# Optimization experiments

Measured on AMD Instinct MI355X. Metric: run time of the kernel, lower is better.

Reference implementation:

```python
import jax, jax.numpy as jnp
import numpy as np

N = 50000
NUM_NEIGHBORS = 16
E = N * NUM_NEIGHBORS
NDIM_IN, EDIM, NDIM_OUT = 128, 64, 128


def setup_inputs() -> dict:
    key = jax.random.key(0)
    k1, k2, k3, k4, k5, k6, k7 = jax.random.split(key, 7)
    nfeats = jax.random.normal(k1, (N, 1, NDIM_IN), dtype=jnp.float32)
    efeats = jax.random.normal(k2, (E, 1, EDIM), dtype=jnp.float32)
    W_msg = jax.random.normal(k3, (NDIM_OUT, NDIM_IN + EDIM), dtype=jnp.float32) * 0.05
    b_msg = jax.random.normal(k4, (NDIM_OUT,), dtype=jnp.float32) * 0.05
    W_apply = jax.random.normal(k5, (NDIM_OUT, NDIM_IN + NDIM_OUT), dtype=jnp.float32) * 0.05
    b_apply = jax.random.normal(k6, (NDIM_OUT,), dtype=jnp.float32) * 0.05
    src_idx = jax.random.randint(k7, (E,), 0, N, dtype=jnp.int32)
    # sampled graph: each node is the destination of exactly NUM_NEIGHBORS edges
    dst_idx = jnp.repeat(jnp.arange(N, dtype=jnp.int32), NUM_NEIGHBORS)
    return {"nfeats": nfeats, "efeats": efeats, "W_msg": W_msg, "b_msg": b_msg,
            "W_apply": W_apply, "b_apply": b_apply, "src_idx": src_idx, "dst_idx": dst_idx}


def reference(nfeats, efeats, W_msg, b_msg, W_apply, b_apply, src_idx, dst_idx):
    n = nfeats.shape[0]
    # message: W_msg(cat([src_h, edge_h], -1))  -> [E, 1, ndim_out]
    src_h = nfeats[src_idx]                                   # [E,1,Din] gather
    msg_in = jnp.concatenate([src_h, efeats], axis=-1)        # [E,1,Din+Edim]
    m = jnp.einsum('eid,od->eio', msg_in, W_msg) + b_msg      # [E,1,Dout]
    # mean aggregation over incoming edges per destination node
    msum = jax.ops.segment_sum(m[:, 0, :], dst_idx, num_segments=n)   # [N,Dout]
    cnt = jax.ops.segment_sum(jnp.ones((m.shape[0],), m.dtype), dst_idx, num_segments=n)
    h_neigh = (msum / jnp.maximum(cnt, 1.0)[:, None])[:, None, :]     # [N,1,Dout]
    # apply: relu(W_apply(cat([nfeats, h_neigh], -1)))
    app_in = jnp.concatenate([nfeats, h_neigh], axis=-1)      # [N,1,Din+Dout]
    h_new = jax.nn.relu(jnp.einsum('nid,od->nio', app_in, W_apply) + b_apply)
    return h_new
```

## Files before the change

### kernel.cpp

```cpp
#include <hip/hip_runtime.h>

#define N_NODES 50000
#define NN 16
#define K_FUSED 320
#define NP 50048

typedef __attribute__((ext_vector_type(8))) short bfrag8;
typedef __attribute__((ext_vector_type(4))) float facc4;

__device__ __forceinline__ unsigned short f2bf(float f) {
    unsigned int u = __builtin_bit_cast(unsigned int, f);
    u = (u + 0x7fffu + ((u >> 16) & 1u)) >> 16;
    return (unsigned short)u;
}

__global__ void wfuse_kernel(const float* __restrict__ W_msg,
                             const float* __restrict__ b_msg,
                             const float* __restrict__ W_apply,
                             const float* __restrict__ b_apply,
                             unsigned short* __restrict__ Wf,
                             float* __restrict__ bias_f) {
    __shared__ float sWa[128];
    const int o = blockIdx.x;
    const int tid = threadIdx.x;
    if (tid < 128) sWa[tid] = W_apply[o * 256 + 128 + tid];
    __syncthreads();
    if (tid < 128) Wf[o * K_FUSED + tid] = f2bf(W_apply[o * 256 + tid]);
    if (tid < 192) {
        float acc = 0.f;
        #pragma unroll 8
        for (int p = 0; p < 128; ++p) acc += sWa[p] * W_msg[p * 192 + tid];
        Wf[o * K_FUSED + 128 + tid] = f2bf(acc);
    } else if (tid == 192) {
        float acc = b_apply[o];
        for (int p = 0; p < 128; ++p) acc += sWa[p] * b_msg[p];
        bias_f[o] = acc;
    }
}

__global__ __launch_bounds__(256)
void prep_kernel(const float* __restrict__ nfeats,
                 const float* __restrict__ efeats,
                 const int* __restrict__ src_idx,
                 unsigned short* __restrict__ X) {
    const int wave = threadIdx.x >> 6;
    const int lane = threadIdx.x & 63;
    const int n = blockIdx.x * 4 + wave;
    if (n >= N_NODES) return;
    const long e0 = (long)n * NN;

    float s0 = 0.f, s1 = 0.f;
    float tacc = 0.f;
    #pragma unroll
    for (int j = 0; j < NN; ++j) {
        const int src = src_idx[e0 + j];
        const float2 v = *(const float2*)(nfeats + (long)src * 128 + 2 * lane);
        s0 += v.x; s1 += v.y;
        tacc += efeats[(e0 + j) * 64 + lane];
    }
    const float inv = 1.f / 16.f;
    s0 *= inv; s1 *= inv; tacc *= inv;

    const float2 xv = *(const float2*)(nfeats + (long)n * 128 + 2 * lane);
    unsigned short* row = X + (long)n * K_FUSED;
    ((unsigned int*)row)[lane] =
        (unsigned)f2bf(xv.x) | ((unsigned)f2bf(xv.y) << 16);
    ((unsigned int*)(row + 128))[lane] =
        (unsigned)f2bf(s0) | ((unsigned)f2bf(s1) << 16);
    row[256 + lane] = f2bf(tacc);
}

__global__ __launch_bounds__(512)
void apply_kernel(const unsigned short* __restrict__ X,
                  const uint4* __restrict__ WfQ,
                  const float* __restrict__ bias_f,
                  float* __restrict__ out) {
    __shared__ uint4 ldsW[64 * 41];
    const int bx = blockIdx.x;
    const int mblk = bx >> 1;
    const int nhalf = bx & 1;
    const int tid = threadIdx.x;

    #pragma unroll
    for (int i = tid; i < 64 * 40; i += 512) {
        const int r = i / 40, q = i - r * 40;
        ldsW[r * 41 + q] = WfQ[(nhalf * 64 + r) * 40 + q];
    }
    __syncthreads();

    const int wave = tid >> 6, lane = tid & 63;
    const int quad = lane >> 4, mcol = lane & 15;
    const int node0 = mblk * 128 + wave * 16;
    const char* arow = (const char*)(X + (long)(node0 + mcol) * K_FUSED);
    const char* ldsB = (const char*)ldsW;

    facc4 acc[4] = {};
    #pragma unroll
    for (int ks = 0; ks < 10; ++ks) {
        const uint4 av = *(const uint4*)(arow + ks * 64 + quad * 16);
        const bfrag8 a = __builtin_bit_cast(bfrag8, av);
        #pragma unroll
        for (int t = 0; t < 4; ++t) {
            const int nrow = t * 16 + mcol;
            const uint4 bv = *(const uint4*)(ldsB + nrow * 656 + ks * 64 + quad * 16);
            const bfrag8 b = __builtin_bit_cast(bfrag8, bv);
            acc[t] = __builtin_amdgcn_mfma_f32_16x16x32_bf16(a, b, acc[t], 0, 0, 0);
        }
    }

    #pragma unroll
    for (int t = 0; t < 4; ++t) {
        const int ocol = nhalf * 64 + t * 16 + mcol;
        const float bb = bias_f[ocol];
        #pragma unroll
        for (int r = 0; r < 4; ++r) {
            const int node = node0 + quad * 4 + r;
            if (node < N_NODES) {
                const float v = acc[t][r] + bb;
                out[(long)node * 128 + ocol] = v > 0.f ? v : 0.f;
            }
        }
    }
}

extern "C" void kernel_launch(void* const* d_in, const int* in_sizes, int n_in,
                              void* d_out, int out_size, void* d_ws, size_t ws_size,
                              hipStream_t stream) {
    const float* nfeats  = (const float*)d_in[0];
    const float* efeats  = (const float*)d_in[1];
    const float* W_msg   = (const float*)d_in[2];
    const float* b_msg   = (const float*)d_in[3];
    const float* W_apply = (const float*)d_in[4];
    const float* b_apply = (const float*)d_in[5];
    const int*   src_idx = (const int*)d_in[6];
    float* out = (float*)d_out;

    char* ws = (char*)d_ws;
    unsigned short* Wf     = (unsigned short*)ws;
    float*          bias_f = (float*)(ws + 81920);
    unsigned short* X      = (unsigned short*)(ws + 82432);

    wfuse_kernel<<<128, 256, 0, stream>>>(W_msg, b_msg, W_apply, b_apply, Wf, bias_f);
    prep_kernel<<<(N_NODES + 3) / 4, 256, 0, stream>>>(nfeats, efeats, src_idx, X);
    apply_kernel<<<(NP / 128) * 2, 512, 0, stream>>>(X, (const uint4*)Wf, bias_f, out);
}
```

Before: 351.5 us.

## Fuse neighbor aggregation into the MFMA apply kernel and gather from bf16 node features

Adds a pre-pass that converts node features to bf16, which halves the bytes moved by the random neighbor gather. The aggregation is now done inside the GEMM kernel: each block builds a 64-row bf16 tile of the aggregated features in LDS, so the intermediate X matrix is no longer written to and read back from global memory. Each wave now computes all 128 output columns, with weights read straight from global/L2 instead of being staged in LDS. The risks are lower occupancy from 8 accumulators, weight loads that are uncoalesced and not cached in LDS, and neighbor sums now built from bf16-rounded inputs.

```diff
diff --git a/kernel.cpp b/kernel.cpp
--- a/kernel.cpp
+++ b/kernel.cpp
@@ -3,7 +3,6 @@
 #define N_NODES 50000
 #define NN 16
 #define K_FUSED 320
-#define NP 50048
 
 typedef __attribute__((ext_vector_type(8))) short bfrag8;
 typedef __attribute__((ext_vector_type(4))) float facc4;
@@ -12,6 +11,12 @@
     unsigned int u = __builtin_bit_cast(unsigned int, f);
     u = (u + 0x7fffu + ((u >> 16) & 1u)) >> 16;
     return (unsigned short)u;
+}
+__device__ __forceinline__ float bflo(unsigned v) {
+    return __builtin_bit_cast(float, v << 16);
+}
+__device__ __forceinline__ float bfhi(unsigned v) {
+    return __builtin_bit_cast(float, v & 0xffff0000u);
 }
 
 __global__ void wfuse_kernel(const float* __restrict__ W_msg,
@@ -39,82 +44,84 @@
 }
 
 __global__ __launch_bounds__(256)
-void prep_kernel(const float* __restrict__ nfeats,
-                 const float* __restrict__ efeats,
-                 const int* __restrict__ src_idx,
-                 unsigned short* __restrict__ X) {
-    const int wave = threadIdx.x >> 6;
-    const int lane = threadIdx.x & 63;
-    const int n = blockIdx.x * 4 + wave;
-    if (n >= N_NODES) return;
-    const long e0 = (long)n * NN;
-
-    float s0 = 0.f, s1 = 0.f;
-    float tacc = 0.f;
-    #pragma unroll
-    for (int j = 0; j < NN; ++j) {
-        const int src = src_idx[e0 + j];
-        const float2 v = *(const float2*)(nfeats + (long)src * 128 + 2 * lane);
-        s0 += v.x; s1 += v.y;
-        tacc += efeats[(e0 + j) * 64 + lane];
-    }
-    const float inv = 1.f / 16.f;
-    s0 *= inv; s1 *= inv; tacc *= inv;
-
-    const float2 xv = *(const float2*)(nfeats + (long)n * 128 + 2 * lane);
-    unsigned short* row = X + (long)n * K_FUSED;
-    ((unsigned int*)row)[lane] =
-        (unsigned)f2bf(xv.x) | ((unsigned)f2bf(xv.y) << 16);
-    ((unsigned int*)(row + 128))[lane] =
-        (unsigned)f2bf(s0) | ((unsigned)f2bf(s1) << 16);
-    row[256 + lane] = f2bf(tacc);
+void nconv_kernel(const float* __restrict__ nf, uint4* __restrict__ nfb) {
+    const long i = (long)blockIdx.x * 256 + threadIdx.x;
+    const float4* p = (const float4*)nf + 2 * i;
+    const float4 a = p[0], b = p[1];
+    uint4 o;
+    o.x = (unsigned)f2bf(a.x) | ((unsigned)f2bf(a.y) << 16);
+    o.y = (unsigned)f2bf(a.z) | ((unsigned)f2bf(a.w) << 16);
+    o.z = (unsigned)f2bf(b.x) | ((unsigned)f2bf(b.y) << 16);
+    o.w = (unsigned)f2bf(b.z) | ((unsigned)f2bf(b.w) << 16);
+    nfb[i] = o;
 }
 
-__global__ __launch_bounds__(512)
-void apply_kernel(const unsigned short* __restrict__ X,
+__global__ __launch_bounds__(256)
+void fused_kernel(const float* __restrict__ efeats,
+                  const int* __restrict__ src_idx,
+                  const unsigned short* __restrict__ nfb,
                   const uint4* __restrict__ WfQ,
                   const float* __restrict__ bias_f,
                   float* __restrict__ out) {
-    __shared__ uint4 ldsW[64 * 41];
-    const int bx = blockIdx.x;
-    const int mblk = bx >> 1;
-    const int nhalf = bx & 1;
+    __shared__ unsigned short Xs[64 * 200];
     const int tid = threadIdx.x;
+    const int wave = tid >> 6, lane = tid & 63;
+    const int nodeBase = blockIdx.x * 64;
 
-    #pragma unroll
-    for (int i = tid; i < 64 * 40; i += 512) {
-        const int r = i / 40, q = i - r * 40;
-        ldsW[r * 41 + q] = WfQ[(nhalf * 64 + r) * 40 + q];
+    for (int nl = 0; nl < 16; ++nl) {
+        const int n = nodeBase + wave * 16 + nl;
+        unsigned short* row = Xs + (wave * 16 + nl) * 200;
+        if (n < N_NODES) {
+            const long e0 = (long)n * NN;
+            float s0 = 0.f, s1 = 0.f, tacc = 0.f;
+            #pragma unroll
+            for (int j = 0; j < NN; ++j) {
+                const int src = src_idx[e0 + j];
+                const unsigned v = *(const unsigned*)(nfb + (long)src * 128 + 2 * lane);
+                s0 += bflo(v); s1 += bfhi(v);
+                tacc += efeats[(e0 + j) * 64 + lane];
+            }
+            const float inv = 1.f / 16.f;
+            ((unsigned*)row)[lane] =
+                (unsigned)f2bf(s0 * inv) | ((unsigned)f2bf(s1 * inv) << 16);
+            row[128 + lane] = f2bf(tacc * inv);
+        } else {
+            ((unsigned*)row)[lane] = 0u;
+            row[128 + lane] = 0;
+        }
     }
     __syncthreads();
 
-    const int wave = tid >> 6, lane = tid & 63;
     const int quad = lane >> 4, mcol = lane & 15;
-    const int node0 = mblk * 128 + wave * 16;
-    const char* arow = (const char*)(X + (long)(node0 + mcol) * K_FUSED);
-    const char* ldsB = (const char*)ldsW;
+    const int nrow = nodeBase + wave * 16 + mcol;
+    const int nclamp = nrow < N_NODES ? nrow : N_NODES - 1;
+    const char* xg = (const char*)(nfb + (long)nclamp * 128);
+    const char* xl = (const char*)(Xs + (wave * 16 + mcol) * 200);
+    const char* wb = (const char*)WfQ;
 
-    facc4 acc[4] = {};
+    facc4 acc[8] = {};
     #pragma unroll
     for (int ks = 0; ks < 10; ++ks) {
-        const uint4 av = *(const uint4*)(arow + ks * 64 + quad * 16);
-        const bfrag8 a = __builtin_bit_cast(bfrag8, av);
+        bfrag8 a;
+        if (ks < 4)
+            a = __builtin_bit_cast(bfrag8, *(const uint4*)(xg + ks * 64 + quad * 16));
+        else
+            a = __builtin_bit_cast(bfrag8, *(const uint4*)(xl + (ks - 4) * 64 + quad * 16));
         #pragma unroll
-        for (int t = 0; t < 4; ++t) {
-            const int nrow = t * 16 + mcol;
-            const uint4 bv = *(const uint4*)(ldsB + nrow * 656 + ks * 64 + quad * 16);
+        for (int t = 0; t < 8; ++t) {
+            const uint4 bv = *(const uint4*)(wb + (t * 16 + mcol) * 640 + ks * 64 + quad * 16);
             const bfrag8 b = __builtin_bit_cast(bfrag8, bv);
             acc[t] = __builtin_amdgcn_mfma_f32_16x16x32_bf16(a, b, acc[t], 0, 0, 0);
         }
     }
 
     #pragma unroll
-    for (int t = 0; t < 4; ++t) {
-        const int ocol = nhalf * 64 + t * 16 + mcol;
+    for (int t = 0; t < 8; ++t) {
+        const int ocol = t * 16 + mcol;
         const float bb = bias_f[ocol];
         #pragma unroll
         for (int r = 0; r < 4; ++r) {
-            const int node = node0 + quad * 4 + r;
+            const int node = nodeBase + wave * 16 + quad * 4 + r;
             if (node < N_NODES) {
                 const float v = acc[t][r] + bb;
                 out[(long)node * 128 + ocol] = v > 0.f ? v : 0.f;
@@ -138,9 +145,10 @@
     char* ws = (char*)d_ws;
     unsigned short* Wf     = (unsigned short*)ws;
     float*          bias_f = (float*)(ws + 81920);
-    unsigned short* X      = (unsigned short*)(ws + 82432);
+    unsigned short* nfb    = (unsigned short*)(ws + 82432);
 
     wfuse_kernel<<<128, 256, 0, stream>>>(W_msg, b_msg, W_apply, b_apply, Wf, bias_f);
-    prep_kernel<<<(N_NODES + 3) / 4, 256, 0, stream>>>(nfeats, efeats, src_idx, X);
-    apply_kernel<<<(NP / 128) * 2, 512, 0, stream>>>(X, (const uint4*)Wf, bias_f, out);
+    nconv_kernel<<<3125, 256, 0, stream>>>(nfeats, (uint4*)nfb);
+    fused_kernel<<<(N_NODES + 63) / 64, 256, 0, stream>>>(
+        efeats, src_idx, nfb, (const uint4*)Wf, bias_f, out);
 }
```

New measurement: 375.3 us. 6.8% more time.
